# Kernel optimization log

Hardware: AMD Instinct MI355X
Metric: run time of the kernel (lower is better)

The kernel has to match this reference:

```python
import jax, jax.numpy as jnp
import numpy as np


def setup_inputs() -> dict:
    key = jax.random.key(0)
    k1, k2, k3, k4 = jax.random.split(key, 4)
    B, S = 4096, 200
    NUM_EMB, EMB_DIM = 512, 64
    INIT_STD = 0.05
    return {
        "input_numeric": jax.random.normal(k1, (B, S, 1), dtype=jnp.float32),
        "proj_w": jax.random.normal(k2, (NUM_EMB, 1), dtype=jnp.float32),
        "proj_b": jax.random.normal(k3, (NUM_EMB,), dtype=jnp.float32),
        "emb_table": jax.random.normal(k4, (NUM_EMB, EMB_DIM), dtype=jnp.float32) * INIT_STD,
    }


def reference(input_numeric, proj_w, proj_b, emb_table):
    # Linear(1 -> num_embeddings): [B,S,1] @ [1,N] + [N] -> [B,S,N]
    logits = input_numeric * proj_w[:, 0] + proj_b
    weights = jax.nn.softmax(logits, axis=-1)  # [B,S,N]
    # (weights.unsqueeze(-1) * emb_table).sum(-2) == weights @ emb_table
    return jnp.einsum("bsn,nd->bsd", weights, emb_table)
```

## Files before the change

### kernel.cpp

```cpp
#include <hip/hip_runtime.h>
#include <stdint.h>

typedef __attribute__((ext_vector_type(8))) short short8;
typedef __attribute__((ext_vector_type(4))) float floatx4;
typedef __attribute__((ext_vector_type(4))) unsigned int uintx4;

static constexpr float kLog2e = 1.4426950408889634f;

__device__ __forceinline__ unsigned short f2bf_rne(float f) {
  uint32_t u = __float_as_uint(f);
  u += 0x7FFFu + ((u >> 16) & 1u);
  return (unsigned short)(u >> 16);
}

__global__ __launch_bounds__(256) void soft_emb_prep(
    const float* __restrict__ emb,
    const float* __restrict__ pw,
    const float* __restrict__ pb,
    unsigned short* __restrict__ etg,
    float2* __restrict__ wbg) {
  const int t = threadIdx.x;
  const int bk = blockIdx.x;
  const int n = t & 63;
  const int k0 = bk * 64 + (t >> 6) * 16;
  #pragma unroll
  for (int i = 0; i < 16; ++i) {
    float v = emb[(size_t)(k0 + i) * 64 + n];
    etg[n * 512 + k0 + i] = f2bf_rne(v);
  }
  if (bk == 0) {
    #pragma unroll
    for (int j = 0; j < 2; ++j) {
      int k = t + j * 256;
      wbg[k] = make_float2(pw[k] * kLog2e, pb[k] * kLog2e);
    }
  }
}

__global__ __launch_bounds__(256, 2) void soft_emb_main(
    const float* __restrict__ x,
    const unsigned short* __restrict__ etg,
    const float2* __restrict__ wbg,
    float* __restrict__ out) {
  __shared__ __align__(16) unsigned short ET[64 * 512];

  const int tid = threadIdx.x;
  {
    const uintx4* g = (const uintx4*)etg;
    uintx4* l = (uintx4*)ET;
    #pragma unroll
    for (int i = 0; i < 16; ++i) l[i * 256 + tid] = g[i * 256 + tid];
  }
  __syncthreads();

  const int lane = tid & 63;
  const int wv = tid >> 6;
  const int n15 = lane & 15;
  const int q = lane >> 4;

  union U8 { uint32_t u[4]; short8 s; };
  U8 ones;
  {
    uint32_t ov = (n15 == 0) ? 0x3F803F80u : 0u;
    ones.u[0] = ones.u[1] = ones.u[2] = ones.u[3] = ov;
  }

  const int base0 = blockIdx.x * 512 + wv * 128;

  #pragma unroll 1
  for (int round = 0; round < 2; ++round) {
    const int tok0 = base0 + round * 64;
    float xv[4];
    #pragma unroll
    for (int t = 0; t < 4; ++t) xv[t] = x[tok0 + t * 16 + n15];

    floatx4 acc[4][4];
    floatx4 accD[4];
    #pragma unroll
    for (int t = 0; t < 4; ++t) {
      accD[t] = floatx4{0.f, 0.f, 0.f, 0.f};
      #pragma unroll
      for (int ti = 0; ti < 4; ++ti) acc[t][ti] = floatx4{0.f, 0.f, 0.f, 0.f};
    }

    #pragma unroll 2
    for (int ks = 0; ks < 16; ++ks) {
      const int kk = ks * 32 + q * 8;

      float4 wbv[4];
      const float4* wp = (const float4*)(wbg + kk);
      #pragma unroll
      for (int jp = 0; jp < 4; ++jp) wbv[jp] = wp[jp];

      short8 bs[4];
      #pragma unroll
      for (int ti = 0; ti < 4; ++ti)
        bs[ti] = *(const short8*)(ET + ((n15 + 16 * ti) << 9) + kk);

      #pragma unroll
      for (int t = 0; t < 4; ++t) {
        U8 A;
        #pragma unroll
        for (int jp = 0; jp < 4; ++jp) {
          float e0 = __builtin_amdgcn_exp2f(fmaf(xv[t], wbv[jp].x, wbv[jp].y));
          float e1 = __builtin_amdgcn_exp2f(fmaf(xv[t], wbv[jp].z, wbv[jp].w));
          A.u[jp] = __builtin_amdgcn_perm(__float_as_uint(e1) + 0x8000u,
                                          __float_as_uint(e0) + 0x8000u,
                                          0x07060302u);
        }
        #pragma unroll
        for (int ti = 0; ti < 4; ++ti)
          acc[t][ti] = __builtin_amdgcn_mfma_f32_16x16x32_bf16(
              A.s, bs[ti], acc[t][ti], 0, 0, 0);
        accD[t] = __builtin_amdgcn_mfma_f32_16x16x32_bf16(
            A.s, ones.s, accD[t], 0, 0, 0);
      }
    }

    #pragma unroll
    for (int t = 0; t < 4; ++t) {
      #pragma unroll
      for (int r = 0; r < 4; ++r) {
        float den = __shfl(accD[t][r], lane & 48, 64);
        float inv = __builtin_amdgcn_rcpf(den);
        float* op = out + (size_t)(tok0 + t * 16 + q * 4 + r) * 64 + n15;
        op[0]  = acc[t][0][r] * inv;
        op[16] = acc[t][1][r] * inv;
        op[32] = acc[t][2][r] * inv;
        op[48] = acc[t][3][r] * inv;
      }
    }
  }
}

extern "C" void kernel_launch(void* const* d_in, const int* in_sizes, int n_in,
                              void* d_out, int out_size, void* d_ws, size_t ws_size,
                              hipStream_t stream) {
  (void)in_sizes; (void)n_in; (void)out_size; (void)ws_size;
  const float* x   = (const float*)d_in[0];
  const float* pw  = (const float*)d_in[1];
  const float* pb  = (const float*)d_in[2];
  const float* emb = (const float*)d_in[3];
  unsigned short* etg = (unsigned short*)d_ws;
  float2* wbg = (float2*)((char*)d_ws + 64 * 512 * 2);
  float* out = (float*)d_out;

  soft_emb_prep<<<8, 256, 0, stream>>>(emb, pw, pb, etg, wbg);
  soft_emb_main<<<1600, 256, 0, stream>>>(x, etg, wbg, out);
}
```

Before: 277.2 us.

## Swizzle LDS embedding layout, pack params for packed FMA, halve per-block work

Stores the transposed bf16 embedding table with an XOR swizzle on 8-element chunks, to remove LDS bank conflicts on the 16-byte B-operand reads. Reorders the weight/bias array as float4 pairs so logits can be computed with packed 2-wide FMA, and uses the library bf16x2 round-to-nearest conversion instead of the manual add-and-perm truncation. Each block now handles 256 tokens in one pass instead of two rounds, with twice as many blocks launched. The cost is that every block still loads the full 64 KB table into LDS, so table-load traffic per token doubles.

```diff
diff --git a/kernel.cpp b/kernel.cpp
--- a/kernel.cpp
+++ b/kernel.cpp
@@ -1,8 +1,10 @@
 #include <hip/hip_runtime.h>
+#include <hip/hip_bf16.h>
 #include <stdint.h>
 
 typedef __attribute__((ext_vector_type(8))) short short8;
 typedef __attribute__((ext_vector_type(4))) float floatx4;
+typedef __attribute__((ext_vector_type(2))) float floatx2;
 typedef __attribute__((ext_vector_type(4))) unsigned int uintx4;
 
 static constexpr float kLog2e = 1.4426950408889634f;
@@ -18,29 +20,28 @@
     const float* __restrict__ pw,
     const float* __restrict__ pb,
     unsigned short* __restrict__ etg,
-    float2* __restrict__ wbg) {
+    float4* __restrict__ wbg4) {
   const int t = threadIdx.x;
   const int bk = blockIdx.x;
   const int n = t & 63;
   const int k0 = bk * 64 + (t >> 6) * 16;
   #pragma unroll
   for (int i = 0; i < 16; ++i) {
-    float v = emb[(size_t)(k0 + i) * 64 + n];
-    etg[n * 512 + k0 + i] = f2bf_rne(v);
+    const int k = k0 + i;
+    float v = emb[(size_t)k * 64 + n];
+    etg[n * 512 + ((((k >> 3) ^ (n & 7)) << 3) | (k & 7))] = f2bf_rne(v);
   }
   if (bk == 0) {
-    #pragma unroll
-    for (int j = 0; j < 2; ++j) {
-      int k = t + j * 256;
-      wbg[k] = make_float2(pw[k] * kLog2e, pb[k] * kLog2e);
-    }
+    const int p = t;
+    wbg4[p] = make_float4(pw[2 * p] * kLog2e, pw[2 * p + 1] * kLog2e,
+                          pb[2 * p] * kLog2e, pb[2 * p + 1] * kLog2e);
   }
 }
 
 __global__ __launch_bounds__(256, 2) void soft_emb_main(
     const float* __restrict__ x,
     const unsigned short* __restrict__ etg,
-    const float2* __restrict__ wbg,
+    const float4* __restrict__ wbg4,
     float* __restrict__ out) {
   __shared__ __align__(16) unsigned short ET[64 * 512];
 
@@ -57,78 +58,85 @@
   const int wv = tid >> 6;
   const int n15 = lane & 15;
   const int q = lane >> 4;
+  const int s = n15 & 7;
 
-  union U8 { uint32_t u[4]; short8 s; };
+  union U8 { uint32_t u[4]; short8 v; };
   U8 ones;
   {
     uint32_t ov = (n15 == 0) ? 0x3F803F80u : 0u;
     ones.u[0] = ones.u[1] = ones.u[2] = ones.u[3] = ov;
   }
 
-  const int base0 = blockIdx.x * 512 + wv * 128;
+  const int tok0 = blockIdx.x * 256 + wv * 64;
 
-  #pragma unroll 1
-  for (int round = 0; round < 2; ++round) {
-    const int tok0 = base0 + round * 64;
-    float xv[4];
+  floatx2 xv2[4];
+  #pragma unroll
+  for (int t = 0; t < 4; ++t) {
+    float xv = x[tok0 + t * 16 + n15];
+    xv2[t] = floatx2{xv, xv};
+  }
+
+  int roff[4];
+  #pragma unroll
+  for (int ti = 0; ti < 4; ++ti) roff[ti] = (n15 + 16 * ti) << 9;
+
+  floatx4 acc[4][4];
+  floatx4 accD[4];
+  #pragma unroll
+  for (int t = 0; t < 4; ++t) {
+    accD[t] = floatx4{0.f, 0.f, 0.f, 0.f};
     #pragma unroll
-    for (int t = 0; t < 4; ++t) xv[t] = x[tok0 + t * 16 + n15];
+    for (int ti = 0; ti < 4; ++ti) acc[t][ti] = floatx4{0.f, 0.f, 0.f, 0.f};
+  }
 
-    floatx4 acc[4][4];
-    floatx4 accD[4];
+  #pragma unroll 2
+  for (int ks = 0; ks < 16; ++ks) {
+    const int kk = ks * 32 + q * 8;
+
+    float4 wbv[4];
+    const float4* wp = wbg4 + (kk >> 1);
     #pragma unroll
-    for (int t = 0; t < 4; ++t) {
-      accD[t] = floatx4{0.f, 0.f, 0.f, 0.f};
-      #pragma unroll
-      for (int ti = 0; ti < 4; ++ti) acc[t][ti] = floatx4{0.f, 0.f, 0.f, 0.f};
-    }
+    for (int jp = 0; jp < 4; ++jp) wbv[jp] = wp[jp];
 
-    #pragma unroll 2
-    for (int ks = 0; ks < 16; ++ks) {
-      const int kk = ks * 32 + q * 8;
-
-      float4 wbv[4];
-      const float4* wp = (const float4*)(wbg + kk);
-      #pragma unroll
-      for (int jp = 0; jp < 4; ++jp) wbv[jp] = wp[jp];
-
-      short8 bs[4];
-      #pragma unroll
-      for (int ti = 0; ti < 4; ++ti)
-        bs[ti] = *(const short8*)(ET + ((n15 + 16 * ti) << 9) + kk);
-
-      #pragma unroll
-      for (int t = 0; t < 4; ++t) {
-        U8 A;
-        #pragma unroll
-        for (int jp = 0; jp < 4; ++jp) {
-          float e0 = __builtin_amdgcn_exp2f(fmaf(xv[t], wbv[jp].x, wbv[jp].y));
-          float e1 = __builtin_amdgcn_exp2f(fmaf(xv[t], wbv[jp].z, wbv[jp].w));
-          A.u[jp] = __builtin_amdgcn_perm(__float_as_uint(e1) + 0x8000u,
-                                          __float_as_uint(e0) + 0x8000u,
-                                          0x07060302u);
-        }
-        #pragma unroll
-        for (int ti = 0; ti < 4; ++ti)
-          acc[t][ti] = __builtin_amdgcn_mfma_f32_16x16x32_bf16(
-              A.s, bs[ti], acc[t][ti], 0, 0, 0);
-        accD[t] = __builtin_amdgcn_mfma_f32_16x16x32_bf16(
-            A.s, ones.s, accD[t], 0, 0, 0);
-      }
-    }
+    const int pc = ((((ks << 2) | q) ^ s) << 3);
+    short8 bs[4];
+    #pragma unroll
+    for (int ti = 0; ti < 4; ++ti)
+      bs[ti] = *(const short8*)(ET + roff[ti] + pc);
 
     #pragma unroll
     for (int t = 0; t < 4; ++t) {
+      U8 A;
       #pragma unroll
-      for (int r = 0; r < 4; ++r) {
-        float den = __shfl(accD[t][r], lane & 48, 64);
-        float inv = __builtin_amdgcn_rcpf(den);
-        float* op = out + (size_t)(tok0 + t * 16 + q * 4 + r) * 64 + n15;
-        op[0]  = acc[t][0][r] * inv;
-        op[16] = acc[t][1][r] * inv;
-        op[32] = acc[t][2][r] * inv;
-        op[48] = acc[t][3][r] * inv;
+      for (int jp = 0; jp < 4; ++jp) {
+        floatx2 l2 = xv2[t] * floatx2{wbv[jp].x, wbv[jp].y}
+                             + floatx2{wbv[jp].z, wbv[jp].w};
+        float e0 = __builtin_amdgcn_exp2f(l2.x);
+        float e1 = __builtin_amdgcn_exp2f(l2.y);
+        union { __hip_bfloat162 h; uint32_t u32; } cv;
+        cv.h = __float22bfloat162_rn(make_float2(e0, e1));
+        A.u[jp] = cv.u32;
       }
+      #pragma unroll
+      for (int ti = 0; ti < 4; ++ti)
+        acc[t][ti] = __builtin_amdgcn_mfma_f32_16x16x32_bf16(
+            A.v, bs[ti], acc[t][ti], 0, 0, 0);
+      accD[t] = __builtin_amdgcn_mfma_f32_16x16x32_bf16(
+          A.v, ones.v, accD[t], 0, 0, 0);
+    }
+  }
+
+  #pragma unroll
+  for (int t = 0; t < 4; ++t) {
+    #pragma unroll
+    for (int r = 0; r < 4; ++r) {
+      float den = __shfl(accD[t][r], lane & 48, 64);
+      float inv = __builtin_amdgcn_rcpf(den);
+      float* op = out + (size_t)(tok0 + t * 16 + q * 4 + r) * 64 + n15;
+      op[0]  = acc[t][0][r] * inv;
+      op[16] = acc[t][1][r] * inv;
+      op[32] = acc[t][2][r] * inv;
+      op[48] = acc[t][3][r] * inv;
     }
   }
 }
@@ -142,9 +150,9 @@
   const float* pb  = (const float*)d_in[2];
   const float* emb = (const float*)d_in[3];
   unsigned short* etg = (unsigned short*)d_ws;
-  float2* wbg = (float2*)((char*)d_ws + 64 * 512 * 2);
+  float4* wbg4 = (float4*)((char*)d_ws + 64 * 512 * 2);
   float* out = (float*)d_out;
 
-  soft_emb_prep<<<8, 256, 0, stream>>>(emb, pw, pb, etg, wbg);
-  soft_emb_main<<<1600, 256, 0, stream>>>(x, etg, wbg, out);
+  soft_emb_prep<<<8, 256, 0, stream>>>(emb, pw, pb, etg, wbg4);
+  soft_emb_main<<<3200, 256, 0, stream>>>(x, etg, wbg4, out);
 }
```

Result: faster. 267.2 us (-3.6%).
